# Kernel optimization log

Hardware: AMD Instinct MI355X
Metric: run time of the kernel (lower is better)

Reference implementation:

```python
import jax, jax.numpy as jnp
import numpy as np
from jax import lax

B, TX, RX, RATE, DIMZ, HID, DIRS = 8192, 32, 32, 2, 64, 128, 2
S, FEAT = 2 * TX, 2 * TX + 1
BN_EPS = 1e-5
GD_STEP = 1e-6   # hardcoded in original forward
GD_ITERS = 10    # hardcoded in original forward


def setup_inputs() -> dict:
    key = jax.random.key(0)
    ks = jax.random.split(key, 9)
    sc = 1.0 / np.sqrt(HID)
    return {
        "y": jax.random.normal(ks[0], (B, 2 * RX), jnp.float32),
        "H": jax.random.normal(ks[1], (B, 2 * RX, 2 * TX), jnp.float32),
        "x_raw": jax.random.randint(ks[2], (B, 2 * TX, 1), 0, 2 ** RATE).astype(jnp.float32),
        "gru_w_ih": jax.random.uniform(ks[3], (DIRS, 3 * HID, FEAT), jnp.float32, -sc, sc),
        "gru_w_hh": jax.random.uniform(ks[4], (DIRS, 3 * HID, HID), jnp.float32, -sc, sc),
        "gru_b_ih": jax.random.uniform(ks[5], (DIRS, 3 * HID), jnp.float32, -sc, sc),
        "gru_b_hh": jax.random.uniform(ks[6], (DIRS, 3 * HID), jnp.float32, -sc, sc),
        "w_Wz": jax.random.normal(ks[7], (DIMZ, DIRS * HID), jnp.float32),
        "w_Wx": jax.random.normal(ks[8], (DIMZ, DIRS * HID), jnp.float32),
        "bn_gamma": jnp.ones((2 * TX,), jnp.float32),
        "bn_beta": jnp.zeros((2 * TX,), jnp.float32),
        "step_size": 1,
        "iterations": 10,
    }


def _gru_dir(x_seq, wih, whh, bih, bhh):
    # x_seq: (S, B, F); PyTorch GRU cell equations
    xg = jnp.einsum('sbf,gf->sbg', x_seq, wih) + bih  # (S, B, 3H)

    def step(h, xg_t):
        hg = h @ whh.T + bhh
        xr, xz, xn = jnp.split(xg_t, 3, axis=-1)
        hr, hz, hn = jnp.split(hg, 3, axis=-1)
        r = jax.nn.sigmoid(xr + hr)
        z = jax.nn.sigmoid(xz + hz)
        n = jnp.tanh(xn + r * hn)
        h = (1.0 - z) * n + z * h
        return h, h

    h0 = jnp.zeros((x_seq.shape[1], whh.shape[1]), x_seq.dtype)
    _, out = lax.scan(step, h0, xg)
    return out  # (S, B, H)


def reference(y, H, x_raw, gru_w_ih, gru_w_hh, gru_b_ih, gru_b_hh,
              w_Wz, w_Wx, bn_gamma, bn_beta, step_size, iterations):
    # Hty: (B, 2tx, 1), HtH: (B, 2tx, 2tx)
    Hty = jnp.einsum('brt,br->bt', H, y)[..., None]
    HtH = jnp.einsum('brt,bru->btu', H, H)

    # BatchNorm1d over channel dim 2tx (stats over batch and last dim)
    feats = jnp.concatenate([HtH, Hty], axis=-1)  # (B, 2tx, 2tx+1)
    mu = feats.mean(axis=(0, 2), keepdims=True)
    var = feats.var(axis=(0, 2), keepdims=True)
    feats = (feats - mu) / jnp.sqrt(var + BN_EPS)
    feats = feats * bn_gamma[None, :, None] + bn_beta[None, :, None]

    # bidirectional GRU over seq dim (seq_len = 2tx)
    x_seq = jnp.transpose(feats, (1, 0, 2))  # (S, B, F)
    fwd = _gru_dir(x_seq, gru_w_ih[0], gru_w_hh[0], gru_b_ih[0], gru_b_hh[0])
    bwd = _gru_dir(x_seq[::-1], gru_w_ih[1], gru_w_hh[1], gru_b_ih[1], gru_b_hh[1])[::-1]
    go = jnp.concatenate([fwd, bwd], axis=-1)  # (S, B, 2H)

    w_z = jnp.transpose(go @ w_Wz.T, (1, 2, 0))  # (B, dim_z, S)
    w_x = jnp.transpose(go @ w_Wx.T, (1, 0, 2))  # (B, S, dim_z)

    x_hat0 = 2.0 * x_raw - (2.0 ** RATE) + 1.0  # QAM symbols
    z0 = w_z @ x_hat0  # (B, dim_z, 1)

    # gradient-descent loop (step_size/iterations args ignored, as in source)
    wxt = jnp.swapaxes(w_x, 1, 2)        # (B, dim_z, 2tx)
    wxt_hty = wxt @ Hty                  # (B, dim_z, 1)
    whhw = wxt @ (HtH @ w_x)             # (B, dim_z, dim_z)
    two_step = 2.0 * GD_STEP

    def gd(zh, _):
        return zh + two_step * (wxt_hty - whhw @ zh), None

    z_hat, _ = lax.scan(gd, z0, None, length=GD_ITERS)
    return w_x @ z_hat  # (B, 2tx, 1)
```

## Files before the change

kernel.cpp:

```cpp
#include <hip/hip_runtime.h>
#include <math.h>


typedef __attribute__((ext_vector_type(8))) short s8v;
typedef __attribute__((ext_vector_type(4))) float f4v;

__device__ __forceinline__ short f2bf(float x) {
  unsigned u = __float_as_uint(x);
  u += 0x7fffu + ((u >> 16) & 1u);
  return (short)(u >> 16);
}
__device__ __forceinline__ float bf2f(short h) {
  return __uint_as_float(((unsigned)(unsigned short)h) << 16);
}
__device__ __forceinline__ void fma4(float4& c, float a, const float4 w) {
  c.x += a*w.x; c.y += a*w.y; c.z += a*w.z; c.w += a*w.w;
}
__device__ __forceinline__ float vget(const float4& v, int i) { return ((const float*)&v)[i]; }

__device__ __forceinline__ void gload16(const void* g, void* l) {
  __builtin_amdgcn_global_load_lds(
      (const __attribute__((address_space(1))) void*)g,
      (__attribute__((address_space(3))) void*)l, 16, 0, 0);
}

#define MFMA(A, B, C) __builtin_amdgcn_mfma_f32_16x16x32_bf16((A), (B), (C), 0, 0, 0)

__global__ __launch_bounds__(256) void k_feats(
    const float* __restrict__ Hm, const float* __restrict__ y,
    short* __restrict__ fragX, float* __restrict__ htyU, float* __restrict__ bnacc)
{
  __shared__ __align__(16) float Hl[64][68];
  __shared__ float yl[64];
  __shared__ float s1[64], s2[64];
  const int b = blockIdx.x;
  const int tid = threadIdx.x;
  const float* Hb = Hm + (size_t)b*4096;
  for (int i = tid; i < 4096; i += 256) Hl[i>>6][i&63] = Hb[i];
  if (tid < 64) { yl[tid] = y[b*64+tid]; s1[tid] = 0.f; s2[tid] = 0.f; }
  __syncthreads();

  if (tid < 64) {
    float acc = 0.f;
    for (int r = 0; r < 64; ++r) acc += Hl[r][tid]*yl[r];
    htyU[tid*8192 + b] = acc;
    atomicAdd(&s1[tid], acc);
    atomicAdd(&s2[tid], acc*acc);
  }
  const int tg = tid & 15, ug = tid >> 4;
  float4 acc4[4];
  acc4[0]=acc4[1]=acc4[2]=acc4[3]=make_float4(0.f,0.f,0.f,0.f);
  for (int r = 0; r < 64; ++r) {
    const float4 tv = *(const float4*)&Hl[r][4*tg];
    const float4 uv = *(const float4*)&Hl[r][4*ug];
    #pragma unroll
    for (int tt=0;tt<4;++tt) fma4(acc4[tt], vget(tv,tt), uv);
  }
  const int mt   = (b >> 4) & 3;
  const int brow = b & 15;
  const int u0   = 4*ug;
  short* fbase = fragX + (size_t)(b >> 6)*64*8192
               + (mt*2 + (u0 >> 5))*512 + (brow + 16*((u0 >> 3) & 3))*8 + (u0 & 7);
  #pragma unroll
  for (int tt=0;tt<4;++tt) {
    const int t = 4*tg+tt;
    float sv=0.f, sq=0.f;
    short hib[4], lob[4];
    #pragma unroll
    for (int uu=0;uu<4;++uu) {
      const float v = vget(acc4[tt],uu);
      const short hi = f2bf(v);
      hib[uu] = hi; lob[uu] = f2bf(v - bf2f(hi));
      sv += v; sq += v*v;
    }
    short* dst = fbase + (size_t)t*8192;
    *(short4*)dst          = make_short4(hib[0],hib[1],hib[2],hib[3]);
    *(short4*)(dst + 4096) = make_short4(lob[0],lob[1],lob[2],lob[3]);
    sv += __shfl_down(sv,32); sq += __shfl_down(sq,32);
    sv += __shfl_down(sv,16); sq += __shfl_down(sq,16);
    if ((tid & 63) < 16) { atomicAdd(&s1[t], sv); atomicAdd(&s2[t], sq); }
  }
  __syncthreads();
  if (tid < 64) {
    atomicAdd(&bnacc[tid*16],      s1[tid]);
    atomicAdd(&bnacc[(64+tid)*16], s2[tid]);
  }
}

__global__ void k_bnfin(const float* __restrict__ bnacc, const float* __restrict__ gam,
                        const float* __restrict__ bet, float* __restrict__ bnac)
{
  const int t = threadIdx.x;
  if (t < 64) {
    const float inv = 1.f/532480.f;
    const float mu  = bnacc[t*16]*inv;
    const float var = bnacc[(64+t)*16]*inv - mu*mu;
    const float a = gam[t]*rsqrtf(var + 1e-5f);
    bnac[t] = a;
    bnac[64+t] = bet[t] - mu*a;
  }
}

__global__ __launch_bounds__(256) void k_prep(
    const float* __restrict__ wih, const float* __restrict__ whh,
    const float* __restrict__ Wz, const float* __restrict__ Wx,
    short* __restrict__ Wg, short* __restrict__ W2g, float* __restrict__ rowsum)
{
  const int i = blockIdx.x*256 + threadIdx.x;
  if (i < 294912) {
    const int dd = i / 147456, r = i % 147456;
    const int sp = r / 73728, r2 = r % 73728;
    const int chunk = r2 / 512, e = r2 % 512;
    const int lane = e >> 3, ii = e & 7;
    const int nt = chunk / 6, kt = chunk % 6;
    const int n = nt*16 + (lane & 15);
    const int k = kt*32 + (lane >> 4)*8 + ii;
    const float v = (k < 64) ? wih[dd*24960 + n*65 + k]
                             : whh[dd*49152 + n*128 + (k - 64)];
    const short hi = f2bf(v);
    Wg[i] = sp ? f2bf(v - bf2f(hi)) : hi;
  } else if (i < 360448) {
    const int t = i - 294912;
    const int dd = t / 32768, r = t % 32768;
    const int sp = r / 16384, r2 = r % 16384;
    const int chunk = r2 / 512, e = r2 % 512;
    const int lane = e >> 3, ii = e & 7;
    const int nt2 = chunk / 4, kt = chunk % 4;
    const int n2 = nt2*16 + (lane & 15);
    const int k = kt*32 + (lane >> 4)*8 + ii;
    const float v = (n2 < 64) ? Wx[n2*256 + dd*128 + k]
                              : Wz[(n2 - 64)*256 + dd*128 + k];
    const short hi = f2bf(v);
    W2g[t] = sp ? f2bf(v - bf2f(hi)) : hi;
  } else if (i < 361216) {
    const int t = i - 360448;
    const int dd = t / 384, g = t % 384;
    float ssum = 0.f;
    for (int f = 0; f < 65; ++f) ssum += wih[dd*24960 + g*65 + f];
    rowsum[t] = ssum;
  }
}

__global__ __launch_bounds__(512, 2) void k_scan(
    const short* __restrict__ fragX, const float* __restrict__ htyU,
    const float* __restrict__ xraw,
    const short* __restrict__ Wg, const short* __restrict__ W2g,
    const float* __restrict__ bih, const float* __restrict__ bhh,
    const float* __restrict__ rowsum, const float* __restrict__ bnac,
    const float* __restrict__ wih,
    float* __restrict__ wx_out, float* __restrict__ z0_out)
{
  __shared__ __align__(16) short Axb[16384];
  __shared__ __align__(16) short Ahb[32768];
  __shared__ __align__(16) float xl[64][68];
  __shared__ __align__(16) float gcl[1536];
  __shared__ __align__(16) float z0l[64][68];
  __shared__ float bna[128];

  const int tid = threadIdx.x;
  const int l   = tid & 63;
  const int w   = __builtin_amdgcn_readfirstlane(tid >> 6);
  const int tile = blockIdx.x >> 1, d = blockIdx.x & 1;
  const int b0  = tile * 64;
  const int l15 = l & 15, lq = l >> 4;
  const int j   = 16*w + l15;
  const int zcol = 16*(w & 3) + l15;

  const short* Wgd = Wg  + d*147456;
  const short* W2d = W2g + d*32768;
  float* wxo = wx_out + (size_t)d * (8192ull*4096ull);
  float* z0o = z0_out + (size_t)d * (8192ull*64ull);

  s8v BR[6][2], BZ[6][2], BN[6][2], BP[4][2];
  #pragma unroll
  for (int kt = 0; kt < 6; ++kt)
    #pragma unroll
    for (int sp = 0; sp < 2; ++sp) {
      BR[kt][sp] = *(const s8v*)&Wgd[((sp*24 + w     )*6 + kt)*512 + l*8];
      BZ[kt][sp] = *(const s8v*)&Wgd[((sp*24 + 8 + w )*6 + kt)*512 + l*8];
      BN[kt][sp] = *(const s8v*)&Wgd[((sp*24 + 16 + w)*6 + kt)*512 + l*8];
    }
  #pragma unroll
  for (int kt = 0; kt < 4; ++kt)
    #pragma unroll
    for (int sp = 0; sp < 2; ++sp)
      BP[kt][sp] = *(const s8v*)&W2d[((sp*8 + w)*4 + kt)*512 + l*8];

  const int hw_base = (j >> 5)*512 + ((j >> 3) & 3)*128 + (j & 7);

  for (int i = tid; i < 32768; i += 512) Ahb[i] = 0;
  for (int i = tid; i < 4096; i += 512) {
    const int bl = i >> 6, s = i & 63;
    xl[s][bl] = 2.f*xraw[(size_t)(b0 + bl)*64 + s] - 3.f;
  }
  if (tid < 128) {
    const int jj = tid;
    float* g = &gcl[jj*12];
    g[0] = rowsum[d*384 + jj];
    g[1] = rowsum[d*384 + 128 + jj];
    g[2] = rowsum[d*384 + 256 + jj];
    g[3] = bih[d*384 + jj]       + bhh[d*384 + jj];
    g[4] = bih[d*384 + 128 + jj] + bhh[d*384 + 128 + jj];
    g[5] = bih[d*384 + 256 + jj];
    g[6] = bhh[d*384 + 256 + jj];
    g[7] = wih[d*24960 + jj*65 + 64];
    g[8] = wih[d*24960 + (128 + jj)*65 + 64];
    g[9] = wih[d*24960 + (256 + jj)*65 + 64];
    g[10] = 0.f; g[11] = 0.f;
  }
  for (int i = tid; i < 64*68; i += 512) ((float*)z0l)[i] = 0.f;
  if (tid < 128) bna[tid] = bnac[tid];

  f4v hprev[4];
  #pragma unroll
  for (int mt = 0; mt < 4; ++mt) hprev[mt] = (f4v)0.f;

  {
    const int s0 = d ? 63 : 0;
    const char* src0 = (const char*)(fragX + (size_t)(tile*64 + s0)*8192);
    char* ax0 = (char*)Axb;
    gload16(src0 + tid*16,        ax0 + w*1024);
    gload16(src0 + 8192 + tid*16, ax0 + 8192 + w*1024);
  }
  __syncthreads();

  for (int it = 0; it < 64; ++it) {
    const int s  = d ? 63 - it : it;
    const int sn = (it < 63) ? (d ? s - 1 : s + 1) : s;

    const short* AxR = Axb + ((it & 1) << 13);
    char*        AxW = (char*)Axb + (((it + 1) & 1) << 14);
    const short* AhR = Ahb + (((it + 1) & 1) << 14);
    short*       AhW = Ahb + ((it & 1) << 14);

    {
      const char* srcn = (const char*)(fragX + (size_t)(tile*64 + sn)*8192);
      gload16(srcn + tid*16,        AxW + w*1024);
      gload16(srcn + 8192 + tid*16, AxW + 8192 + w*1024);
    }

    const float a_s = bna[s], c_s = bna[64 + s];
    const volatile float* gj = gcl + j*12;
    const float crK  = c_s*gj[0] + gj[3];
    const float czK  = c_s*gj[1] + gj[4];
    const float cnK  = c_s*gj[2] + gj[5];
    const float BHN  = gj[6];
    const float w64r = gj[7], w64z = gj[8], w64n = gj[9];

    #pragma unroll
    for (int mt = 0; mt < 4; ++mt) {
      const float4 av4 = *(const float4*)&htyU[s*8192 + b0 + mt*16 + lq*4];
      f4v Crx = (f4v)0.f, Czx = (f4v)0.f, Cnx = (f4v)0.f;
      f4v Crh = (f4v)0.f, Czh = (f4v)0.f, Cnh = (f4v)0.f;
      #pragma unroll
      for (int kt = 0; kt < 2; ++kt) {
        const s8v axh = *(const s8v*)&AxR[mt*1024 + kt*512 + l*8];
        const s8v axl = *(const s8v*)&AxR[4096 + mt*1024 + kt*512 + l*8];
        Crx = MFMA(axh, BR[kt][0], Crx); Crx = MFMA(axh, BR[kt][1], Crx); Crx = MFMA(axl, BR[kt][0], Crx);
        Czx = MFMA(axh, BZ[kt][0], Czx); Czx = MFMA(axh, BZ[kt][1], Czx); Czx = MFMA(axl, BZ[kt][0], Czx);
        Cnx = MFMA(axh, BN[kt][0], Cnx); Cnx = MFMA(axh, BN[kt][1], Cnx); Cnx = MFMA(axl, BN[kt][0], Cnx);
      }
      #pragma unroll
      for (int kh = 0; kh < 4; ++kh) {
        const s8v ahh = *(const s8v*)&AhR[mt*2048 + kh*512 + l*8];
        const s8v ahl = *(const s8v*)&AhR[8192 + mt*2048 + kh*512 + l*8];
        const int kt = 2 + kh;
        Crh = MFMA(ahh, BR[kt][0], Crh); Crh = MFMA(ahh, BR[kt][1], Crh); Crh = MFMA(ahl, BR[kt][0], Crh);
        Czh = MFMA(ahh, BZ[kt][0], Czh); Czh = MFMA(ahh, BZ[kt][1], Czh); Czh = MFMA(ahl, BZ[kt][0], Czh);
        Cnh = MFMA(ahh, BN[kt][0], Cnh); Cnh = MFMA(ahh, BN[kt][1], Cnh); Cnh = MFMA(ahl, BN[kt][0], Cnh);
      }
      f4v av; av[0]=av4.x; av[1]=av4.y; av[2]=av4.z; av[3]=av4.w;
      Crx += av * w64r; Czx += av * w64z; Cnx += av * w64n;
      #pragma unroll
      for (int e = 0; e < 4; ++e) {
        const float rr  = 1.f/(1.f + __expf(-(a_s*Crx[e] + Crh[e] + crK)));
        const float zz  = 1.f/(1.f + __expf(-(a_s*Czx[e] + Czh[e] + czK)));
        const float pre = a_s*Cnx[e] + cnK + rr*(Cnh[e] + BHN);
        const float ax2 = fabsf(pre);
        const float ee  = __expf(-2.f*ax2);
        const float nn  = copysignf((1.f - ee)/(1.f + ee), pre);
        hprev[mt][e] = (1.f - zz)*nn + zz*hprev[mt][e];
      }
    }

    #pragma unroll
    for (int mt = 0; mt < 4; ++mt)
      #pragma unroll
      for (int e = 0; e < 4; ++e) {
        const float hv = hprev[mt][e];
        const short hi = f2bf(hv);
        const int ad = mt*2048 + hw_base + (lq*4 + e)*8;
        AhW[ad] = hi;
        AhW[8192 + ad] = f2bf(hv - bf2f(hi));
      }
    __syncthreads();

    #pragma unroll
    for (int mt = 0; mt < 4; ++mt) {
      f4v Cp = (f4v)0.f;
      #pragma unroll
      for (int kt = 0; kt < 4; ++kt) {
        const s8v ahh = *(const s8v*)&AhW[mt*2048 + kt*512 + l*8];
        const s8v ahl = *(const s8v*)&AhW[8192 + mt*2048 + kt*512 + l*8];
        Cp = MFMA(ahh, BP[kt][0], Cp);
        Cp = MFMA(ahh, BP[kt][1], Cp);
        Cp = MFMA(ahl, BP[kt][0], Cp);
      }
      if (w < 4) {
        #pragma unroll
        for (int e = 0; e < 4; ++e)
          wxo[(size_t)(b0 + mt*16 + lq*4 + e)*4096 + s*64 + 16*w + l15] = Cp[e];
      } else {
        #pragma unroll
        for (int e = 0; e < 4; ++e) {
          const int bl = mt*16 + lq*4 + e;
          z0l[bl][zcol] += xl[s][bl] * Cp[e];
        }
      }
    }
  }
  if (w >= 4) {
    #pragma unroll
    for (int mt = 0; mt < 4; ++mt)
      #pragma unroll
      for (int e = 0; e < 4; ++e) {
        const int bl = mt*16 + lq*4 + e;
        z0o[(size_t)(b0 + bl)*64 + zcol] = z0l[bl][zcol];
      }
  }
}

__global__ __launch_bounds__(256) void k_gd(
    const float* __restrict__ Hm, const float* __restrict__ y,
    const float* __restrict__ wxf, const float* __restrict__ wxb,
    const float* __restrict__ z0f, const float* __restrict__ z0b,
    float* __restrict__ out)
{
  __shared__ __align__(16) float Hl[64][68];
  __shared__ __align__(16) float wx[64][68];
  __shared__ __align__(16) float tmp[64][68];
  __shared__ float yl[64], wh[64], zv[64];
  const int b = blockIdx.x;
  const int tid = threadIdx.x;
  const float* Hb = Hm + (size_t)b*4096;
  for (int i = tid; i < 4096; i += 256) {
    Hl[i>>6][i&63] = Hb[i];
    wx[i>>6][i&63] = wxf[(size_t)b*4096 + i] + wxb[(size_t)b*4096 + i];
  }
  if (tid < 64) {
    yl[tid] = y[b*64+tid];
    zv[tid] = z0f[(size_t)b*64+tid] + z0b[(size_t)b*64+tid];
  }
  __syncthreads();
  const int zq = tid & 15, tq = tid >> 4;
  #pragma unroll
  for (int rr = 0; rr < 4; ++rr) {
    const int r = 4*tq + rr;
    float4 a = make_float4(0.f,0.f,0.f,0.f);
    for (int t = 0; t < 64; ++t) fma4(a, Hl[r][t], *(const float4*)&wx[t][4*zq]);
    *(float4*)&tmp[r][4*zq] = a;
  }
  __syncthreads();
  float (*ww)[68] = Hl;
  #pragma unroll
  for (int ii = 0; ii < 4; ++ii) {
    const int zi = 4*tq + ii;
    float4 a = make_float4(0.f,0.f,0.f,0.f);
    for (int r = 0; r < 64; ++r) fma4(a, tmp[r][zi], *(const float4*)&tmp[r][4*zq]);
    *(float4*)&ww[zi][4*zq] = a;
  }
  if (tid < 64) {
    float acc = 0.f;
    for (int r = 0; r < 64; ++r) acc += tmp[r][tid]*yl[r];
    wh[tid] = acc;
  }
  __syncthreads();
  for (int itr = 0; itr < 10; ++itr) {
    float nz = 0.f;
    if (tid < 64) {
      float mv = 0.f;
      for (int k2 = 0; k2 < 64; ++k2) mv += ww[tid][k2]*zv[k2];
      nz = zv[tid] + 2e-6f*(wh[tid] - mv);
    }
    __syncthreads();
    if (tid < 64) zv[tid] = nz;
    __syncthreads();
  }
  if (tid < 64) {
    float o = 0.f;
    for (int z2 = 0; z2 < 64; ++z2) o += wx[tid][z2]*zv[z2];
    out[(size_t)b*64 + tid] = o;
  }
}

extern "C" void kernel_launch(void* const* d_in, const int* in_sizes, int n_in,
                              void* d_out, int out_size, void* d_ws, size_t ws_size,
                              hipStream_t stream)
{
  const float* y    = (const float*)d_in[0];
  const float* Hm   = (const float*)d_in[1];
  const float* xraw = (const float*)d_in[2];
  const float* wih  = (const float*)d_in[3];
  const float* whh  = (const float*)d_in[4];
  const float* bih  = (const float*)d_in[5];
  const float* bhh  = (const float*)d_in[6];
  const float* Wz   = (const float*)d_in[7];
  const float* Wx   = (const float*)d_in[8];
  const float* gam  = (const float*)d_in[9];
  const float* bet  = (const float*)d_in[10];
  float* out = (float*)d_out;
  float* ws  = (float*)d_ws;

  float* wxf   = ws;
  float* wxb   = wxf + 33554432ull;
  float* z0f   = wxb + 33554432ull;
  float* z0b   = z0f + 524288ull;
  float* htyU  = z0b + 524288ull;
  float* rows  = htyU + 524288ull;
  float* bnacc = rows + 768ull;
  float* bnac  = bnacc + 2048ull;
  short* Wgs   = (short*)(bnac + 128ull);
  short* W2gs  = Wgs + 294912ull;
  short* fragX = W2gs + 65536ull;

  hipMemsetAsync(bnacc, 0, 2048*sizeof(float), stream);
  k_feats <<<8192, 256, 0, stream>>>(Hm, y, fragX, htyU, bnacc);
  k_prep  <<<1412, 256, 0, stream>>>(wih, whh, Wz, Wx, Wgs, W2gs, rows);
  k_bnfin <<<1, 64, 0, stream>>>(bnacc, gam, bet, bnac);
  k_scan  <<<256, 512, 0, stream>>>(fragX, htyU, xraw, Wgs, W2gs,
                                    bih, bhh, rows, bnac, wih, wxf, z0f);
  k_gd    <<<8192, 256, 0, stream>>>(Hm, y, wxf, wxb, z0f, z0b, out);
}
```

Before: 2.167 ms.

## Prefetch GRU input fragments two steps ahead and stage Hty in LDS

The loads of the per-step input fragments are rescheduled so that the next-but-one step's fragment is fetched right after the mid-iteration barrier into the buffer just consumed. This gives each async global-to-LDS load a full iteration to land. The barrier becomes a manual s_waitcnt plus s_barrier, with a partial vmcnt wait on waves 0-3 so they do not stall on their outstanding output stores. Hty values are also copied once into shared memory instead of being read from global memory every step. The hand-written waitcnt counts are fragile and depend on how many stores the compiler has in flight, and the extra 17 KB of LDS may reduce occupancy.

```diff
diff --git a/kernel.cpp b/kernel.cpp
--- a/kernel.cpp
+++ b/kernel.cpp
@@ -153,6 +153,7 @@
   __shared__ __align__(16) short Axb[16384];
   __shared__ __align__(16) short Ahb[32768];
   __shared__ __align__(16) float xl[64][68];
+  __shared__ __align__(16) float htyl[64][68];
   __shared__ __align__(16) float gcl[1536];
   __shared__ __align__(16) float z0l[64][68];
   __shared__ float bna[128];
@@ -192,6 +193,10 @@
   for (int i = tid; i < 4096; i += 512) {
     const int bl = i >> 6, s = i & 63;
     xl[s][bl] = 2.f*xraw[(size_t)(b0 + bl)*64 + s] - 3.f;
+  }
+  for (int i = tid; i < 4096; i += 512) {
+    const int s = i >> 6, bl = i & 63;
+    htyl[s][bl] = htyU[s*8192 + b0 + bl];
   }
   if (tid < 128) {
     const int jj = tid;
@@ -217,27 +222,24 @@
 
   {
     const int s0 = d ? 63 : 0;
+    const int s1 = d ? 62 : 1;
     const char* src0 = (const char*)(fragX + (size_t)(tile*64 + s0)*8192);
+    const char* src1 = (const char*)(fragX + (size_t)(tile*64 + s1)*8192);
     char* ax0 = (char*)Axb;
+    char* ax1 = (char*)Axb + 16384;
     gload16(src0 + tid*16,        ax0 + w*1024);
     gload16(src0 + 8192 + tid*16, ax0 + 8192 + w*1024);
+    gload16(src1 + tid*16,        ax1 + w*1024);
+    gload16(src1 + 8192 + tid*16, ax1 + 8192 + w*1024);
   }
   __syncthreads();
 
   for (int it = 0; it < 64; ++it) {
-    const int s  = d ? 63 - it : it;
-    const int sn = (it < 63) ? (d ? s - 1 : s + 1) : s;
+    const int s = d ? 63 - it : it;
 
     const short* AxR = Axb + ((it & 1) << 13);
-    char*        AxW = (char*)Axb + (((it + 1) & 1) << 14);
     const short* AhR = Ahb + (((it + 1) & 1) << 14);
     short*       AhW = Ahb + ((it & 1) << 14);
-
-    {
-      const char* srcn = (const char*)(fragX + (size_t)(tile*64 + sn)*8192);
-      gload16(srcn + tid*16,        AxW + w*1024);
-      gload16(srcn + 8192 + tid*16, AxW + 8192 + w*1024);
-    }
 
     const float a_s = bna[s], c_s = bna[64 + s];
     const volatile float* gj = gcl + j*12;
@@ -249,7 +251,6 @@
 
     #pragma unroll
     for (int mt = 0; mt < 4; ++mt) {
-      const float4 av4 = *(const float4*)&htyU[s*8192 + b0 + mt*16 + lq*4];
       f4v Crx = (f4v)0.f, Czx = (f4v)0.f, Cnx = (f4v)0.f;
       f4v Crh = (f4v)0.f, Czh = (f4v)0.f, Cnh = (f4v)0.f;
       #pragma unroll
@@ -269,6 +270,7 @@
         Czh = MFMA(ahh, BZ[kt][0], Czh); Czh = MFMA(ahh, BZ[kt][1], Czh); Czh = MFMA(ahl, BZ[kt][0], Czh);
         Cnh = MFMA(ahh, BN[kt][0], Cnh); Cnh = MFMA(ahh, BN[kt][1], Cnh); Cnh = MFMA(ahl, BN[kt][0], Cnh);
       }
+      const float4 av4 = *(const float4*)&htyl[s][mt*16 + lq*4];
       f4v av; av[0]=av4.x; av[1]=av4.y; av[2]=av4.z; av[3]=av4.w;
       Crx += av * w64r; Czx += av * w64z; Cnx += av * w64n;
       #pragma unroll
@@ -293,7 +295,24 @@
         AhW[ad] = hi;
         AhW[8192 + ad] = f2bf(hv - bf2f(hi));
       }
-    __syncthreads();
+
+    __builtin_amdgcn_sched_barrier(0);
+    if (w < 4) {
+      asm volatile("s_waitcnt vmcnt(16) lgkmcnt(0)" ::: "memory");
+    } else {
+      asm volatile("s_waitcnt vmcnt(0) lgkmcnt(0)" ::: "memory");
+    }
+    __builtin_amdgcn_s_barrier();
+    __builtin_amdgcn_sched_barrier(0);
+
+    if (it < 62) {
+      const int sn2 = d ? 61 - it : it + 2;
+      const char* srcn = (const char*)(fragX + (size_t)(tile*64 + sn2)*8192);
+      char* AxW = (char*)Axb + ((it & 1) << 14);
+      gload16(srcn + tid*16,        AxW + w*1024);
+      gload16(srcn + 8192 + tid*16, AxW + 8192 + w*1024);
+    }
+    __builtin_amdgcn_sched_barrier(0);
 
     #pragma unroll
     for (int mt = 0; mt < 4; ++mt) {
```

After: 2.141 ms. Within noise of the previous version (-1.2%).
